# Kernel optimization log

Measured on AMD Instinct MI355X. Metric: run time of the kernel, lower is better.

Reference implementation:

```python
import jax, jax.numpy as jnp
import numpy as np

B, C, H, W = 4, 128, 96, 96
E = 4
C8 = C // 8


def _conv1x1(w, b, x):
    # w: [out, in], x: [b, in, H, W]
    return jnp.einsum('oi,bihw->bohw', w, x) + b[None, :, None, None]


def _bilinear_zeros(x, gx, gy):
    # x: [b, C, h, w]; gx, gy: [b, H2, W2] normalized coords in [-1, 1]
    # align_corners=True, padding_mode='zeros' (matches F.grid_sample)
    b, c, h, w = x.shape
    ix = (gx + 1.0) * 0.5 * (w - 1)
    iy = (gy + 1.0) * 0.5 * (h - 1)
    ix0 = jnp.floor(ix)
    iy0 = jnp.floor(iy)
    tx = ix - ix0
    ty = iy - iy0
    ix0 = ix0.astype(jnp.int32)
    iy0 = iy0.astype(jnp.int32)

    def gather(yy, xx):
        valid = ((xx >= 0) & (xx < w) & (yy >= 0) & (yy < h)).astype(x.dtype)
        xc = jnp.clip(xx, 0, w - 1)
        yc = jnp.clip(yy, 0, h - 1)
        vals = jax.vmap(lambda xb, y, xi: xb[:, y, xi])(x, yc, xc)  # [b,C,H2,W2]
        return vals * valid[:, None]

    w00 = ((1 - tx) * (1 - ty))[:, None]
    w01 = (tx * (1 - ty))[:, None]
    w10 = ((1 - tx) * ty)[:, None]
    w11 = (tx * ty)[:, None]
    return (gather(iy0, ix0) * w00 + gather(iy0, ix0 + 1) * w01
            + gather(iy0 + 1, ix0) * w10 + gather(iy0 + 1, ix0 + 1) * w11)


def setup_inputs() -> dict:
    key = jax.random.key(0)
    ks = jax.random.split(key, 12)
    s = 0.05
    return {
        'x': jax.random.normal(ks[0], (B, C, H, W), jnp.float32),
        'weight_compress': jax.random.normal(ks[1], (E, C8, C), jnp.float32) * s,
        'weight_expand': jax.random.normal(ks[2], (E, C, C8), jnp.float32) * s,
        'body_w1': jax.random.normal(ks[3], (64, 3), jnp.float32) * s,
        'body_b1': jax.random.normal(ks[4], (64,), jnp.float32) * s,
        'body_w2': jax.random.normal(ks[5], (64, 64), jnp.float32) * s,
        'body_b2': jax.random.normal(ks[6], (64,), jnp.float32) * s,
        'rout_w': jax.random.normal(ks[7], (E, 64), jnp.float32) * s,
        'rout_b': jax.random.normal(ks[8], (E,), jnp.float32) * s,
        'off_w': jax.random.normal(ks[9], (2, 64), jnp.float32) * s,
        'off_b': jax.random.normal(ks[10], (2,), jnp.float32) * s,
        'scale': 2,
    }


def reference(x, weight_compress, weight_expand, body_w1, body_b1,
              body_w2, body_b2, rout_w, rout_b, off_w, off_b, scale):
    b, c, h, w = x.shape
    sc = float(scale)
    H2 = round(h * sc)
    W2 = round(w * sc)

    # fractional sub-pixel coordinates (meta-upsample positional encoding)
    ch = (jnp.arange(H2, dtype=jnp.float32) + 0.5) / sc
    ch = ch - jnp.floor(ch + 0.001) - 0.5  # [H2]
    cw = (jnp.arange(W2, dtype=jnp.float32) + 0.5) / sc
    cw = cw - jnp.floor(cw + 0.001) - 0.5  # [W2]
    inp = jnp.stack([
        jnp.full((H2, W2), 1.0 / sc, jnp.float32),
        jnp.broadcast_to(ch[:, None], (H2, W2)),
        jnp.broadcast_to(cw[None, :], (H2, W2)),
    ], axis=0)[None]  # [1, 3, H2, W2]

    emb = jax.nn.relu(_conv1x1(body_w1, body_b1, inp))
    emb = jax.nn.relu(_conv1x1(body_w2, body_b2, emb))
    offset = _conv1x1(off_w, off_b, emb)                      # [1, 2, H2, W2]
    routing = jax.nn.sigmoid(_conv1x1(rout_w, rout_b, emb))   # [1, E, H2, W2]
    r = routing[0].transpose(1, 2, 0)                         # [H2, W2, E]

    # base sampling grid, align_corners=True normalization + learned offset
    gx = ((jnp.arange(W2, dtype=jnp.float32) + 0.5) / sc - 0.5) * 2.0 / (w - 1) - 1.0
    gy = ((jnp.arange(H2, dtype=jnp.float32) + 0.5) / sc - 0.5) * 2.0 / (h - 1) - 1.0
    gx = gx[None, None, :] + offset[:, 0] * 2.0 / (w - 1)     # [1, H2, W2]
    gy = gy[None, :, None] + offset[:, 1] * 2.0 / (h - 1)
    gx = jnp.broadcast_to(gx, (b, H2, W2))
    gy = jnp.broadcast_to(gy, (b, H2, W2))

    fea0 = _bilinear_zeros(x, gx, gy)          # [b, C, H2, W2]
    fea = fea0.transpose(0, 2, 3, 1)           # [b, H2, W2, C]

    # per-pixel routed 1x1 convs: compress (C->C/8) then expand (C/8->C)
    comp = jnp.einsum('bhwc,hwe,eoc->bhwo', fea, r, weight_compress)
    out = jnp.einsum('bhwo,hwe,eco->bhwc', comp, r, weight_expand)
    return out.transpose(0, 3, 1, 2) + fea0
```

## Files before the change

### kernel.cpp

```cpp
#include <hip/hip_runtime.h>
#include <math.h>

#define Bn 4
#define Cc 128
#define Hh 96
#define Ww 96
#define H2c 192
#define W2c 192
#define HW (Hh*Ww)

#define WC_OFF 0
#define WE_OFF (4*2048)
#define TAP_OFF (8*2048)
#define M_OFF  16640

typedef float  f32x4  __attribute__((ext_vector_type(4)));
typedef short  s16x8  __attribute__((ext_vector_type(8)));

__device__ __forceinline__ unsigned f2bf(float f) {
    unsigned u = __float_as_uint(f);
    return (u + 0x7FFFu + ((u >> 16) & 1u)) >> 16;
}

__global__ __launch_bounds__(256) void k1_mix(
    const float* __restrict__ wcomp, const float* __restrict__ wexp,
    const float* __restrict__ bw1, const float* __restrict__ bb1,
    const float* __restrict__ bw2, const float* __restrict__ bb2,
    const float* __restrict__ rw,  const float* __restrict__ rb,
    const float* __restrict__ ow,  const float* __restrict__ ob,
    float* __restrict__ ws)
{
    __shared__ float e1[64], e2[64], rr[4], of[2];
    const int tid   = threadIdx.x;
    const int cls   = blockIdx.x >> 4;
    const int chunk = blockIdx.x & 15;
    const float chv = (cls & 2) ? 0.25f : -0.25f;
    const float cwv = (cls & 1) ? 0.25f : -0.25f;

    if (tid < 64) {
        float h = bw1[tid*3+0]*0.5f + bw1[tid*3+1]*chv + bw1[tid*3+2]*cwv + bb1[tid];
        e1[tid] = fmaxf(h, 0.f);
    }
    __syncthreads();
    if (tid < 64) {
        float s = bb2[tid];
        for (int i = 0; i < 64; ++i) s += bw2[tid*64+i]*e1[i];
        e2[tid] = fmaxf(s, 0.f);
    }
    __syncthreads();
    if (tid < 6) {
        if (tid < 4) {
            float s = rb[tid];
            for (int i = 0; i < 64; ++i) s += rw[tid*64+i]*e2[i];
            rr[tid] = 1.f/(1.f+expf(-s));
        } else {
            const int d = tid - 4;
            float s = ob[d];
            for (int i = 0; i < 64; ++i) s += ow[d*64+i]*e2[i];
            of[d] = s;
        }
    }
    __syncthreads();
    const float r0 = rr[0], r1 = rr[1], r2 = rr[2], r3 = rr[3];

    if (tid < 128) {
        const int idx = chunk*128 + tid;
        const int o = idx >> 7, c = idx & 127;
        const float v = r0*wcomp[idx] + r1*wcomp[2048+idx]
                      + r2*wcomp[4096+idx] + r3*wcomp[6144+idx];
        ws[WC_OFF + cls*2048 + c*16 + o] = v;
    } else {
        const int idx = chunk*128 + (tid - 128);
        ws[WE_OFF + cls*2048 + idx] =
            r0*wexp[idx] + r1*wexp[2048+idx] + r2*wexp[4096+idx] + r3*wexp[6144+idx];
    }
    if (chunk == 0 && tid == 0) {
        const float fx = cwv + of[0];
        const float fy = chv + of[1];
        const float Dx = floorf(fx), Dy = floorf(fy);
        ws[TAP_OFF + cls*4 + 0] = fx - Dx;
        ws[TAP_OFF + cls*4 + 1] = fy - Dy;
        ws[TAP_OFF + cls*4 + 2] = Dx;
        ws[TAP_OFF + cls*4 + 3] = Dy;
    }
}

__global__ __launch_bounds__(256) void k1b_fold(
    const float* __restrict__ wsr, unsigned short* __restrict__ Mw)
{
    const int t   = blockIdx.x*256 + threadIdx.x;
    const int cls = t >> 12;
    const int rem = t & 4095;
    const int co  = rem >> 5;
    const int ci0 = (rem & 31) * 4;
    const float* we = wsr + WE_OFF + cls*2048 + co*16;

    float m[4];
    #pragma unroll
    for (int q = 0; q < 4; ++q) {
        const float* wc = wsr + WC_OFF + cls*2048 + (ci0+q)*16;
        float s = 0.f;
        #pragma unroll
        for (int o = 0; o < 16; ++o) s += we[o]*wc[o];
        if (co == ci0 + q) s += 1.f;
        m[q] = s;
    }
    uint2 v;
    v.x = f2bf(m[0]) | (f2bf(m[1]) << 16);
    v.y = f2bf(m[2]) | (f2bf(m[3]) << 16);
    *reinterpret_cast<uint2*>(Mw + (size_t)cls*16384 + co*128 + ci0) = v;
}

__device__ __forceinline__ void remap_axis(int c0, int last, float w0, float w1,
                                           int& base, float& a0, float& a1)
{
    base = min(max(c0, 0), last - 1);
    if (c0 >= 0 && c0 < last) { a0 = w0;  a1 = w1;  }
    else if (c0 == -1)        { a0 = w1;  a1 = 0.f; }
    else if (c0 == last)      { a0 = 0.f; a1 = w0;  }
    else                      { a0 = 0.f; a1 = 0.f; }
}

__global__ __launch_bounds__(256) void k2_mfma(
    const float* __restrict__ x, const float* __restrict__ wsr,
    const unsigned short* __restrict__ Mw, float* __restrict__ out)
{
    __shared__ __align__(16) unsigned short lF[64*128];

    const int tid = threadIdx.x;
    const int xl  = tid & 63;
    const int grp = tid >> 6;

    const int n = blockIdx.x;
    const int w = (n & 7) * 288 + (n >> 3);
    const int px_ = w & 1, py = (w >> 1) & 1;
    const int w2 = w >> 2;
    const int tile = w2 % 144;
    const int b    = w2 / 144;
    const int cls  = (py << 1) | px_;

    const unsigned short* Mc = Mw + (size_t)cls*16384;
    s16x8 a[2][4];
    #pragma unroll
    for (int t = 0; t < 2; ++t)
        #pragma unroll
        for (int kk = 0; kk < 4; ++kk) {
            const int row = 32*grp + 16*t + (xl & 15);
            a[t][kk] = *reinterpret_cast<const s16x8*>(
                Mc + row*128 + kk*32 + (xl >> 4)*8);
        }

    const int pix = tile*64 + xl;
    const int j = pix / 96;
    const int i = pix - j*96;

    const float tx = wsr[TAP_OFF + cls*4 + 0];
    const float ty = wsr[TAP_OFF + cls*4 + 1];
    const int   Dx = (int)wsr[TAP_OFF + cls*4 + 2];
    const int   Dy = (int)wsr[TAP_OFF + cls*4 + 3];
    int cb, rbw; float ax0, ax1, ay0, ay1;
    remap_axis(i + Dx, Ww - 1, 1.f - tx, tx, cb,  ax0, ax1);
    remap_axis(j + Dy, Hh - 1, 1.f - ty, ty, rbw, ay0, ay1);
    const float w00 = ay0*ax0, w01 = ay0*ax1, w10 = ay1*ax0, w11 = ay1*ax1;
    const float* xb = x + (size_t)b*Cc*HW + rbw*Ww + cb;

    #pragma unroll
    for (int h = 0; h < 2; ++h) {
        float t00[16], t01[16], t10[16], t11[16];
        #pragma unroll
        for (int k = 0; k < 16; ++k) {
            const float* p = xb + (size_t)(grp*32 + h*16 + k)*HW;
            t00[k] = p[0];
            t01[k] = p[1];
            t10[k] = p[Ww];
            t11[k] = p[Ww+1];
        }
        #pragma unroll
        for (int k = 0; k < 16; k += 4) {
            const float f0 = w00*t00[k  ] + w01*t01[k  ] + w10*t10[k  ] + w11*t11[k  ];
            const float f1 = w00*t00[k+1] + w01*t01[k+1] + w10*t10[k+1] + w11*t11[k+1];
            const float f2 = w00*t00[k+2] + w01*t01[k+2] + w10*t10[k+2] + w11*t11[k+2];
            const float f3 = w00*t00[k+3] + w01*t01[k+3] + w10*t10[k+3] + w11*t11[k+3];
            uint2 v;
            v.x = f2bf(f0) | (f2bf(f1) << 16);
            v.y = f2bf(f2) | (f2bf(f3) << 16);
            const int c = grp*32 + h*16 + k;
            int byte = xl*256 + c*2;
            byte ^= (xl & 7) << 4;
            *reinterpret_cast<uint2*>(reinterpret_cast<char*>(lF) + byte) = v;
        }
    }
    __syncthreads();

    f32x4 acc[2][4];
    #pragma unroll
    for (int t = 0; t < 2; ++t)
        #pragma unroll
        for (int nn = 0; nn < 4; ++nn) acc[t][nn] = (f32x4){0.f, 0.f, 0.f, 0.f};

    #pragma unroll
    for (int kk = 0; kk < 4; ++kk) {
        #pragma unroll
        for (int nn = 0; nn < 4; ++nn) {
            int byte = (nn*16 + (xl & 15))*256 + kk*64 + (xl >> 4)*16;
            byte ^= (xl & 7) << 4;
            const s16x8 bf = *reinterpret_cast<const s16x8*>(
                reinterpret_cast<const char*>(lF) + byte);
            acc[0][nn] = __builtin_amdgcn_mfma_f32_16x16x32_bf16(a[0][kk], bf, acc[0][nn], 0, 0, 0);
            acc[1][nn] = __builtin_amdgcn_mfma_f32_16x16x32_bf16(a[1][kk], bf, acc[1][nn], 0, 0, 0);
        }
    }

    #pragma unroll
    for (int t = 0; t < 2; ++t)
        #pragma unroll
        for (int nn = 0; nn < 4; ++nn) {
            const int pix2 = tile*64 + nn*16 + (xl & 15);
            const int j2 = pix2 / 96;
            const int i2 = pix2 - j2*96;
            const int yg = 2*j2 + py;
            const int xg = 2*i2 + px_;
            const int ch0 = 32*grp + 16*t + (xl >> 4)*4;
            float* op = out + ((size_t)(b*Cc + ch0)*H2c + yg)*W2c + xg;
            #pragma unroll
            for (int r = 0; r < 4; ++r)
                op[(size_t)r*(H2c*W2c)] = acc[t][nn][r];
        }
}

extern "C" void kernel_launch(void* const* d_in, const int* in_sizes, int n_in,
                              void* d_out, int out_size, void* d_ws, size_t ws_size,
                              hipStream_t stream) {
    const float* x     = (const float*)d_in[0];
    const float* wcomp = (const float*)d_in[1];
    const float* wexp  = (const float*)d_in[2];
    const float* bw1   = (const float*)d_in[3];
    const float* bb1   = (const float*)d_in[4];
    const float* bw2   = (const float*)d_in[5];
    const float* bb2   = (const float*)d_in[6];
    const float* rw    = (const float*)d_in[7];
    const float* rb    = (const float*)d_in[8];
    const float* ow    = (const float*)d_in[9];
    const float* ob    = (const float*)d_in[10];
    float* out = (float*)d_out;
    float* ws  = (float*)d_ws;
    unsigned short* Mw = (unsigned short*)(ws + M_OFF);

    k1_mix<<<64, 256, 0, stream>>>(wcomp, wexp, bw1, bb1, bw2, bb2, rw, rb, ow, ob, ws);
    k1b_fold<<<64, 256, 0, stream>>>(ws, Mw);
    k2_mfma<<<2304, 256, 0, stream>>>(x, ws, Mw, out);
}
```

Before: 51.10 us.

## Stage bilinear source windows in LDS via direct global-to-LDS loads

New measurement: 42.97 us. -15.9%, faster.

```diff
diff --git a/kernel.cpp b/kernel.cpp
--- a/kernel.cpp
+++ b/kernel.cpp
@@ -8,6 +8,7 @@
 #define H2c 192
 #define W2c 192
 #define HW (Hh*Ww)
+#define HW2 (H2c*W2c)
 
 #define WC_OFF 0
 #define WE_OFF (4*2048)
@@ -20,6 +21,13 @@
 __device__ __forceinline__ unsigned f2bf(float f) {
     unsigned u = __float_as_uint(f);
     return (u + 0x7FFFu + ((u >> 16) & 1u)) >> 16;
+}
+
+__device__ __forceinline__ void gload_lds16(const float* g, float* l) {
+    __builtin_amdgcn_global_load_lds(
+        (const __attribute__((address_space(1))) unsigned int*)g,
+        (__attribute__((address_space(3))) unsigned int*)l,
+        16, 0, 0);
 }
 
 __global__ __launch_bounds__(256) void k1_mix(
@@ -126,69 +134,89 @@
     const unsigned short* __restrict__ Mw, float* __restrict__ out)
 {
     __shared__ __align__(16) unsigned short lF[64*128];
+    __shared__ __align__(16) float lWin[4*2048];
 
     const int tid = threadIdx.x;
     const int xl  = tid & 63;
     const int grp = tid >> 6;
 
     const int n = blockIdx.x;
-    const int w = (n & 7) * 288 + (n >> 3);
-    const int px_ = w & 1, py = (w >> 1) & 1;
-    const int w2 = w >> 2;
-    const int tile = w2 % 144;
-    const int b    = w2 / 144;
-    const int cls  = (py << 1) | px_;
+    const int w = (n & 7)*288 + (n >> 3);
+    const int cls  = w & 3;
+    const int px_  = cls & 1, py = (cls >> 1) & 1;
+    const int rest = w >> 2;
+    const int tile = rest % 144;
+    const int b    = rest / 144;
+    const int jt = tile/3, xs = tile - jt*3;
+    const int j0 = jt*2, i0 = xs*32;
 
     const unsigned short* Mc = Mw + (size_t)cls*16384;
+    const int lo = xl & 15, hi = xl >> 4;
     s16x8 a[2][4];
     #pragma unroll
     for (int t = 0; t < 2; ++t)
         #pragma unroll
-        for (int kk = 0; kk < 4; ++kk) {
-            const int row = 32*grp + 16*t + (xl & 15);
+        for (int kk = 0; kk < 4; ++kk)
             a[t][kk] = *reinterpret_cast<const s16x8*>(
-                Mc + row*128 + kk*32 + (xl >> 4)*8);
-        }
-
-    const int pix = tile*64 + xl;
-    const int j = pix / 96;
-    const int i = pix - j*96;
+                Mc + (32*grp + 16*t + lo)*128 + kk*32 + hi*8);
+
+    const int pr = xl >> 5, pc = xl & 31;
+    const int j = j0 + pr, i = i0 + pc;
 
     const float tx = wsr[TAP_OFF + cls*4 + 0];
     const float ty = wsr[TAP_OFF + cls*4 + 1];
     const int   Dx = (int)wsr[TAP_OFF + cls*4 + 2];
     const int   Dy = (int)wsr[TAP_OFF + cls*4 + 3];
-    int cb, rbw; float ax0, ax1, ay0, ay1;
-    remap_axis(i + Dx, Ww - 1, 1.f - tx, tx, cb,  ax0, ax1);
-    remap_axis(j + Dy, Hh - 1, 1.f - ty, ty, rbw, ay0, ay1);
+    int basex, basey; float ax0, ax1, ay0, ay1;
+    remap_axis(i + Dx, Ww - 1, 1.f - tx, tx, basex, ax0, ax1);
+    remap_axis(j + Dy, Hh - 1, 1.f - ty, ty, basey, ay0, ay1);
     const float w00 = ay0*ax0, w01 = ay0*ax1, w10 = ay1*ax0, w11 = ay1*ax1;
-    const float* xb = x + (size_t)b*Cc*HW + rbw*Ww + cb;
+
+    const int c0  = i0 + Dx;
+    const int cs0 = min(max(0, c0 & ~3), Ww - 40);
+    const int cidx = basex - cs0;
+    const int ro0 = pr*40 + cidx;
+    const int ro1 = ro0 + 40;
+
+    const int jD = j0 + Dy;
+    const int sl = xl & 31;
+    const int s2 = min(sl, 29);
+    const int lr = s2 / 10, lq = s2 - lr*10;
+    const int lrow = min(max(jD + lr, 0), Hh - 1);
+    const float* gsrc = x + (size_t)b*Cc*HW + (size_t)lrow*Ww + cs0 + 4*lq;
+    const int chsub = xl >> 5;
+
+    float* winw = lWin + grp*2048;
 
     #pragma unroll
     for (int h = 0; h < 2; ++h) {
-        float t00[16], t01[16], t10[16], t11[16];
-        #pragma unroll
-        for (int k = 0; k < 16; ++k) {
-            const float* p = xb + (size_t)(grp*32 + h*16 + k)*HW;
-            t00[k] = p[0];
-            t01[k] = p[1];
-            t10[k] = p[Ww];
-            t11[k] = p[Ww+1];
-        }
-        #pragma unroll
-        for (int k = 0; k < 16; k += 4) {
-            const float f0 = w00*t00[k  ] + w01*t01[k  ] + w10*t10[k  ] + w11*t11[k  ];
-            const float f1 = w00*t00[k+1] + w01*t01[k+1] + w10*t10[k+1] + w11*t11[k+1];
-            const float f2 = w00*t00[k+2] + w01*t01[k+2] + w10*t10[k+2] + w11*t11[k+2];
-            const float f3 = w00*t00[k+3] + w01*t01[k+3] + w10*t10[k+3] + w11*t11[k+3];
+        #pragma unroll
+        for (int p = 0; p < 8; ++p) {
+            const int ch = grp*32 + h*16 + p*2 + chsub;
+            gload_lds16(gsrc + (size_t)ch*HW, winw + p*256);
+        }
+        asm volatile("s_waitcnt vmcnt(0)" ::: "memory");
+        __builtin_amdgcn_sched_barrier(0);
+        #pragma unroll
+        for (int cq = 0; cq < 4; ++cq) {
+            float f[4];
+            #pragma unroll
+            for (int u = 0; u < 4; ++u) {
+                const float* wc = winw + (cq*4 + u)*128;
+                f[u] = w00*wc[ro0] + w01*wc[ro0+1] + w10*wc[ro1] + w11*wc[ro1+1];
+            }
             uint2 v;
-            v.x = f2bf(f0) | (f2bf(f1) << 16);
-            v.y = f2bf(f2) | (f2bf(f3) << 16);
-            const int c = grp*32 + h*16 + k;
+            v.x = f2bf(f[0]) | (f2bf(f[1]) << 16);
+            v.y = f2bf(f[2]) | (f2bf(f[3]) << 16);
+            const int c = grp*32 + h*16 + cq*4;
             int byte = xl*256 + c*2;
             byte ^= (xl & 7) << 4;
             *reinterpret_cast<uint2*>(reinterpret_cast<char*>(lF) + byte) = v;
         }
+        if (h == 0) {
+            asm volatile("s_waitcnt lgkmcnt(0)" ::: "memory");
+            __builtin_amdgcn_sched_barrier(0);
+        }
     }
     __syncthreads();
 
@@ -202,8 +230,8 @@
     for (int kk = 0; kk < 4; ++kk) {
         #pragma unroll
         for (int nn = 0; nn < 4; ++nn) {
-            int byte = (nn*16 + (xl & 15))*256 + kk*64 + (xl >> 4)*16;
-            byte ^= (xl & 7) << 4;
+            int byte = (nn*16 + lo)*256 + kk*64 + hi*16;
+            byte ^= (lo & 7) << 4;
             const s16x8 bf = *reinterpret_cast<const s16x8*>(
                 reinterpret_cast<const char*>(lF) + byte);
             acc[0][nn] = __builtin_amdgcn_mfma_f32_16x16x32_bf16(a[0][kk], bf, acc[0][nn], 0, 0, 0);
@@ -215,16 +243,15 @@
     for (int t = 0; t < 2; ++t)
         #pragma unroll
         for (int nn = 0; nn < 4; ++nn) {
-            const int pix2 = tile*64 + nn*16 + (xl & 15);
-            const int j2 = pix2 / 96;
-            const int i2 = pix2 - j2*96;
-            const int yg = 2*j2 + py;
-            const int xg = 2*i2 + px_;
-            const int ch0 = 32*grp + 16*t + (xl >> 4)*4;
+            const int slot2 = nn*16 + lo;
+            const int pr2 = slot2 >> 5, pc2 = slot2 & 31;
+            const int yg = 2*(j0 + pr2) + py;
+            const int xg = 2*(i0 + pc2) + px_;
+            const int ch0 = 32*grp + 16*t + hi*4;
             float* op = out + ((size_t)(b*Cc + ch0)*H2c + yg)*W2c + xg;
             #pragma unroll
             for (int r = 0; r < 4; ++r)
-                op[(size_t)r*(H2c*W2c)] = acc[t][nn][r];
+                op[(size_t)r*HW2] = acc[t][nn][r];
         }
 }
 
```
